# Kernel optimization log

Measured on AMD Instinct MI355X. Metric: run time of the kernel, lower is better.

The kernel has to match this reference:

```python
import jax, jax.numpy as jnp
import numpy as np

DIM = 6
S = 2 ** DIM  # 64 nonzero B-spline basis products per edge (degree-1 spline)


def _bits():
    # [S, DIM] binary offsets enumerating the 2^dim corners of the spline cell
    return jnp.asarray(((np.arange(S)[:, None] >> np.arange(DIM)[None, :]) & 1).astype(np.int32))


def spline_basis(u, ks):
    # u: [E, DIM] pseudo-coords in [0,1); open B-spline, degree 1
    bits = _bits()                      # [S, DIM]
    v = u * (ks - 1)                    # [E, DIM]
    lo = jnp.floor(v)
    frac = v - lo                       # fractional position in cell
    lo = lo.astype(jnp.int32)
    # basis[e,s] = prod_d (frac if bit else 1-frac)
    basis = jnp.prod(jnp.where(bits[None].astype(bool), frac[:, None, :], 1.0 - frac[:, None, :]), axis=-1)  # [E,S]
    pos = jnp.clip(lo[:, None, :] + bits[None, :, :], 0, ks - 1)  # [E,S,DIM]
    strides = (ks ** jnp.arange(DIM)).astype(jnp.int32)           # per-dim stride in flattened kernel
    idx = jnp.sum(pos * strides[None, None, :], axis=-1)          # [E,S] in [0, ks^DIM)
    return basis, idx


def spline_conv(x, src, dst, basis, idx, W, Wr, b, n):
    # x:[N,in], W:[K,in,out], basis/idx:[E,S]. Mean aggregation + root weight + bias (PyG defaults).
    x_src = x[src]                                  # [E,in] gather
    out_ch = W.shape[2]
    acc0 = jnp.zeros((x_src.shape[0], out_ch), x.dtype)

    def body(acc, bs_is):
        bs, ii = bs_is                              # [E], [E]
        m = jnp.einsum('ei,eio->eo', x_src, W[ii])  # basis-indexed weight gather + per-edge matvec
        return acc + bs[:, None] * m, None

    msg, _ = jax.lax.scan(body, acc0, (basis.T, idx.T))   # loop over S=64 spline corners
    agg = jax.ops.segment_sum(msg, dst, num_segments=n)   # scatter-add to target nodes
    deg = jax.ops.segment_sum(jnp.ones(dst.shape, x.dtype), dst, num_segments=n)
    agg = agg / jnp.clip(deg, 1.0)[:, None]                # aggr='mean'
    return agg + x @ Wr + b


def setup_inputs() -> dict:
    key = jax.random.key(0)
    ks = jax.random.split(key, 16)
    N, E = 4096, 16384
    x = jax.random.normal(ks[0], (N, 32), jnp.float32)
    edge_index = jax.random.randint(ks[1], (2, E), 0, N, jnp.int32)
    edge_attr = jax.random.uniform(ks[2], (E, DIM), jnp.float32)

    def wk(k, K, cin, cout):
        return jax.random.normal(k, (K, cin, cout), jnp.float32) * (1.0 / np.sqrt(cin * S))

    def wr(k, cin, cout):
        return jax.random.normal(k, (cin, cout), jnp.float32) * (1.0 / np.sqrt(cin))

    return {
        'x': x, 'edge_index': edge_index, 'edge_attr': edge_attr,
        'W1': wk(ks[3], 3 ** DIM, 32, 128), 'Wr1': wr(ks[4], 32, 128), 'b1': jnp.zeros((128,), jnp.float32),
        'W3': wk(ks[5], 3 ** DIM, 128, 128), 'Wr3': wr(ks[6], 128, 128), 'b3': jnp.zeros((128,), jnp.float32),
        'W6': wk(ks[7], 5 ** DIM, 128, 64), 'Wr6': wr(ks[8], 128, 64), 'b6': jnp.zeros((64,), jnp.float32),
        'W7': wk(ks[9], 7 ** DIM, 64, 13), 'Wr7': wr(ks[10], 64, 13), 'b7': jnp.zeros((13,), jnp.float32),
    }


def reference(x, edge_index, edge_attr, W1, Wr1, b1, W3, Wr3, b3, W6, Wr6, b6, W7, Wr7, b7):
    src, dst = edge_index[0], edge_index[1]
    n = x.shape[0]
    basis3, idx3 = spline_basis(edge_attr, 3)  # shared by conv1 and conv3 (same kernel_size)
    h = spline_conv(x, src, dst, basis3, idx3, W1, Wr1, b1, n)
    h = spline_conv(h, src, dst, basis3, idx3, W3, Wr3, b3, n)
    basis5, idx5 = spline_basis(edge_attr, 5)
    h = spline_conv(h, src, dst, basis5, idx5, W6, Wr6, b6, n)
    basis7, idx7 = spline_basis(edge_attr, 7)
    h = spline_conv(h, src, dst, basis7, idx7, W7, Wr7, b7, n)
    h = jax.nn.elu(h)
    return jax.nn.log_softmax(h, axis=1)
```

## Files before the change

### kernel.cpp

```cpp
#include <hip/hip_runtime.h>
#include <hip/hip_bf16.h>
#include <cstdint>
#include <cstddef>

constexpr int SDIM = 6;
constexpr int SCOR = 64;
constexpr int CAP5 = 512;
constexpr int CAP7 = 128;
typedef unsigned short u16;
typedef unsigned char u8;
typedef __attribute__((ext_vector_type(8))) short bf16x8;
typedef __attribute__((ext_vector_type(4))) float f32x4;
typedef __attribute__((ext_vector_type(2))) float f32x2;
typedef __attribute__((ext_vector_type(4))) int i32x4;

__device__ __forceinline__ float bf2f(u16 h) {
    union { unsigned u; float f; } v; v.u = ((unsigned)h) << 16; return v.f;
}
__device__ __forceinline__ u16 f2bf(float f) {
    union { float f; unsigned u; } v; v.f = f;
    unsigned r = v.u + 0x7fffu + ((v.u >> 16) & 1u);
    return (u16)(r >> 16);
}

__device__ __forceinline__ u8 f2e4m3(float f) {
#if __has_builtin(__builtin_amdgcn_cvt_pk_fp8_f32)
    return (u8)(__builtin_amdgcn_cvt_pk_fp8_f32(f, 0.0f, 0, false) & 0xff);
#else
    unsigned u = __float_as_uint(f);
    unsigned s = (u >> 24) & 0x80;
    int exp = (int)((u >> 23) & 0xff) - 127;
    unsigned man = u & 0x7fffff;
    if (exp > 8 || (exp == 8 && man >= 0x700000)) return (u8)(s | 0x7e);
    if (exp >= -6) {
        unsigned m = man >> 20;
        unsigned rest = man & 0xfffff;
        if (rest > 0x80000 || (rest == 0x80000 && (m & 1))) m++;
        unsigned v = (((unsigned)(exp + 7)) << 3) + m;
        if (v > 0x7e) v = 0x7e;
        return (u8)(s | v);
    }
    if (exp < -10) return (u8)s;
    float af = __uint_as_float(u & 0x7fffffff);
    int M = (int)(af * 512.0f + 0.5f);
    if (M > 7) M = 7;
    return (u8)(s | M);
#endif
}

__device__ __forceinline__ void e4m3x4_acc(unsigned w, float* a) {
#if __has_builtin(__builtin_amdgcn_cvt_pk_f32_fp8)
    f32x2 lo = __builtin_amdgcn_cvt_pk_f32_fp8((int)w, false);
    f32x2 hi = __builtin_amdgcn_cvt_pk_f32_fp8((int)w, true);
    a[0] += lo.x; a[1] += lo.y; a[2] += hi.x; a[3] += hi.y;
#else
    #pragma unroll
    for (int j = 0; j < 4; j++) {
        unsigned b = (w >> (8 * j)) & 0xff;
        unsigned s = (b & 0x80) << 24;
        unsigned em = b & 0x7f;
        float v = (em >= 8)
            ? __uint_as_float((((em >> 3) + 120) << 23) | ((em & 7) << 20))
            : (float)em * (1.0f / 512.0f);
        a[j] += __uint_as_float(__float_as_uint(v) | s);
    }
#endif
}

template <int KS>
__device__ __forceinline__ void keybasis(const float* u, int s, int& key, float& basis) {
    int idx = 0, str = 1;
    float b = 1.0f;
    #pragma unroll
    for (int d = 0; d < SDIM; d++) {
        float v = u[d] * (KS - 1);
        float fl = floorf(v);
        float fr = v - fl;
        int bit = (s >> d) & 1;
        int pos = (int)fl + bit;
        pos = min(max(pos, 0), KS - 1);
        idx += pos * str;
        str *= KS;
        b *= bit ? fr : (1.0f - fr);
    }
    key = idx;
    basis = b;
}

__global__ __launch_bounds__(256) void prep_kernel(int* __restrict__ zb, int nz,
                                                   const float* __restrict__ xin,
                                                   u16* __restrict__ xbf, int n4) {
    int i = blockIdx.x * blockDim.x + threadIdx.x;
    if (i < nz) zb[i] = 0;
    if (i < n4) {
        float4 v = ((const float4*)xin)[i];
        ushort4 o;
        o.x = f2bf(v.x); o.y = f2bf(v.y); o.z = f2bf(v.z); o.w = f2bf(v.w);
        ((ushort4*)xbf)[i] = o;
    }
}

__global__ __launch_bounds__(256) void count_all(const float* __restrict__ ea,
                                                 const int* __restrict__ dst,
                                                 int* __restrict__ cnt3r,
                                                 int* __restrict__ degi, int P) {
    int gid = blockIdx.x * blockDim.x + threadIdx.x;
    if (gid >= P) return;
    int e = gid >> 6, s = gid & 63;
    int rep = blockIdx.x & 7;
    float u[SDIM];
    #pragma unroll
    for (int d = 0; d < SDIM; d++) u[d] = ea[e * SDIM + d];
    int k; float b;
    keybasis<3>(u, s, k, b);
    atomicAdd(&cnt3r[k * 8 + rep], 1);
    if (s == 0) atomicAdd(&degi[dst[e]], 1);
}

__global__ __launch_bounds__(256) void scan_partial(const int* __restrict__ zb,
                                                    int* __restrict__ bsum) {
    int b = blockIdx.x, t = threadIdx.x;
    int4 v = *(const int4*)(zb + b * 1024 + t * 4);
    __shared__ int red[256];
    red[t] = v.x + v.y + v.z + v.w;
    __syncthreads();
    for (int h = 128; h >= 1; h >>= 1) {
        if (t < h) red[t] += red[t + h];
        __syncthreads();
    }
    if (t == 0) bsum[b] = red[0];
}

__global__ __launch_bounds__(256) void scan_final(int* __restrict__ zb,
                                                  const int* __restrict__ bsum,
                                                  int* __restrict__ eoff,
                                                  int* __restrict__ offs3f,
                                                  int Nn, int nb0) {
    int b = blockIdx.x, t = threadIdx.x;
    int s1 = nb0;
    int seg = (b >= s1) ? 1 : 0;
    int sb = seg ? s1 : 0;
    int L = seg ? 5832 : Nn;
    int* offs = seg ? offs3f : eoff;

    __shared__ int red[256];
    int cnt = b - sb;
    int acc = 0;
    for (int j = t; j < cnt; j += 256) acc += bsum[sb + j];
    red[t] = acc;
    __syncthreads();
    for (int h = 128; h >= 1; h >>= 1) {
        if (t < h) red[t] += red[t + h];
        __syncthreads();
    }
    int blockPrefix = red[0];
    __syncthreads();

    int idx = b * 1024 + t * 4;
    int4 v = *(const int4*)(zb + idx);
    int tsum = v.x + v.y + v.z + v.w;
    __shared__ int ss[256];
    ss[t] = tsum;
    __syncthreads();
    for (int off = 1; off < 256; off <<= 1) {
        int val = (t >= off) ? ss[t - off] : 0;
        __syncthreads();
        ss[t] += val;
        __syncthreads();
    }
    int p = blockPrefix + ((t == 0) ? 0 : ss[t - 1]);
    int pe[4];
    pe[0] = p;
    pe[1] = p + v.x;
    pe[2] = pe[1] + v.y;
    pe[3] = pe[2] + v.z;
    int vv[4] = {v.x, v.y, v.z, v.w};
    int li = (b - sb) * 1024 + t * 4;
    #pragma unroll
    for (int j = 0; j < 4; j++) {
        int gi = li + j;
        if (gi < L) {
            offs[gi] = pe[j];
            zb[idx + j] = pe[j];
            if (gi == L - 1) offs[L] = pe[j] + vv[j];
        }
    }
}

__global__ __launch_bounds__(256) void fill_all(const float* __restrict__ ea,
                                                const int* __restrict__ src,
                                                const int* __restrict__ dst,
                                                int* __restrict__ ecur,
                                                int* __restrict__ cur3r, int2* __restrict__ pP3,
                                                int* __restrict__ cnt5, int2* __restrict__ pP5,
                                                int* __restrict__ cnt7, int2* __restrict__ pP7,
                                                int P) {
    int gid = blockIdx.x * blockDim.x + threadIdx.x;
    if (gid >= P) return;
    int e = gid >> 6;
    int lane = threadIdx.x & 63;
    int rep = blockIdx.x & 7;
    float u[SDIM];
    #pragma unroll
    for (int d = 0; d < SDIM; d++) u[d] = ea[e * SDIM + d];
    int node = src[e];
    int er = 0;
    if (lane == 0) er = atomicAdd(&ecur[dst[e]], 1);
    er = __shfl(er, 0);
    int packed = (node << 20) | (er * SCOR + lane);
    int k; float b; int slot;
    keybasis<3>(u, lane, k, b);
    slot = atomicAdd(&cur3r[k * 8 + rep], 1);
    pP3[slot] = make_int2(packed, __float_as_int(b));
    keybasis<5>(u, lane, k, b);
    slot = k * CAP5 + atomicAdd(&cnt5[k], 1);
    pP5[slot] = make_int2(packed, __float_as_int(b));
    keybasis<7>(u, lane, k, b);
    slot = k * CAP7 + atomicAdd(&cnt7[k], 1);
    pP7[slot] = make_int2(packed, __float_as_int(b));
}

template <int IN, int OUT, int WAVES, int WN, int GY, int OSTR, int CAP>
__global__ __launch_bounds__(WAVES * 64) void conv_mfma_r(
    const u16* __restrict__ xbf, const float* __restrict__ W,
    const int* __restrict__ offs, const int2* __restrict__ pairP,
    u8* __restrict__ mpart) {
    constexpr int NT = WAVES * 64;
    constexpr int WM = WAVES / WN;
    constexpr int OUT16 = (OUT + 15) & ~15;
    static_assert(OUT == OUT16, "conv_mfma_r requires OUT multiple of 16");
    constexpr int WSTR = OUT + 2;
    constexpr int NF = OUT16 / 16;
    constexpr int NFW = NF / WN;
    constexpr int KS = IN / 32;
    constexpr int TW = NFW * 16;
    constexpr int TSTR = TW + 16;
    constexpr int CHW = TW / 16;
    static_assert(TSTR % 16 == 0, "row stride must be 16B aligned");
    static_assert((IN * OUT) % NT == 0, "staging divisibility");

    __shared__ u16 Wlds[IN * WSTR];
    __shared__ u8 tall[WAVES][16 * TSTR];

    int k = blockIdx.x;
    int p0, p1;
    if constexpr (CAP > 0) {
        p0 = k * CAP;
        p1 = p0 + offs[k];
    } else {
        p0 = offs[k * OSTR];
        p1 = offs[(k + 1) * OSTR];
    }
    int t = threadIdx.x;
    int wid = t >> 6, lane = t & 63;
    int wm = wid % WM, wn = wid / WM;
    int l15 = lane & 15, l4 = lane >> 4;
    u8* twave = tall[wid];

    if (p0 + (int)blockIdx.y * WM * 16 >= p1) return;

    const float* Wg = W + (size_t)k * IN * OUT;
    #pragma unroll
    for (int f0 = 0; f0 < IN * OUT; f0 += NT) {
        int f = f0 + t;
        int i = f / OUT, o = f % OUT;
        Wlds[i * WSTR + o] = f2bf(Wg[f]);
    }
    __syncthreads();

    bf16x8 breg[KS][NFW];
    #pragma unroll
    for (int ks = 0; ks < KS; ks++) {
        #pragma unroll
        for (int nf = 0; nf < NFW; nf++) {
            int col = (wn * NFW + nf) * 16 + l15;
            int rbase = ks * 32 + l4 * 8;
            bf16x8 b;
            #pragma unroll
            for (int j = 0; j < 8; j++)
                ((u16*)&b)[j] = Wlds[(rbase + j) * WSTR + col];
            breg[ks][nf] = b;
        }
    }

    constexpr int STRIDE = WM * GY * 16;
    int t0 = p0 + ((int)blockIdx.y * WM + wm) * 16;
    if (t0 >= p1) return;

    int2 meta = pairP[min(t0 + l15, p1 - 1)];
    bf16x8 a[KS];
    {
        const u16* xrow = xbf + (size_t)((unsigned)meta.x >> 20) * IN + l4 * 8;
        #pragma unroll
        for (int ks = 0; ks < KS; ks++) a[ks] = *(const bf16x8*)(xrow + ks * 32);
    }

    while (true) {
        int np = min(16, p1 - t0);
        float basv = (l15 < np) ? __int_as_float(meta.y) * 64.0f : 0.0f;
        int srv = meta.x & 0xFFFFF;
        int tn = t0 + STRIDE;
        bool has = tn < p1;
        int2 metaN = meta;
        if (has) metaN = pairP[min(tn + l15, p1 - 1)];

        f32x4 acc[NFW];
        #pragma unroll
        for (int nf = 0; nf < NFW; nf++)
            acc[nf] = f32x4{0.f, 0.f, 0.f, 0.f};
        #pragma unroll
        for (int ks = 0; ks < KS; ks++) {
            #pragma unroll
            for (int nf = 0; nf < NFW; nf++)
                acc[nf] = __builtin_amdgcn_mfma_f32_16x16x32_bf16(a[ks], breg[ks][nf], acc[nf], 0, 0, 0);
        }

        bf16x8 aN[KS];
        if (has) {
            const u16* xrowN = xbf + (size_t)((unsigned)metaN.x >> 20) * IN + l4 * 8;
            #pragma unroll
            for (int ks = 0; ks < KS; ks++) aN[ks] = *(const bf16x8*)(xrowN + ks * 32);
        }

        #pragma unroll
        for (int nf = 0; nf < NFW; nf++) {
            #pragma unroll
            for (int r = 0; r < 4; r++) {
                int pl = l4 * 4 + r;
                float bs = __shfl(basv, pl);
                twave[pl * TSTR + nf * 16 + l15] = f2e4m3(acc[nf][r] * bs);
            }
        }

        #pragma unroll
        for (int it = 0; it < (16 * CHW + 63) / 64; it++) {
            int cid = it * 64 + lane;
            int row = cid / CHW, ch = cid % CHW;
            int srr = __shfl(srv, row);
            if (cid < 16 * CHW && row < np)
                __builtin_nontemporal_store(
                    *(const i32x4*)&twave[row * TSTR + ch * 16],
                    (i32x4*)(mpart + (size_t)srr * OUT16 + wn * TW + ch * 16));
        }

        if (!has) break;
        t0 = tn;
        meta = metaN;
        #pragma unroll
        for (int ks = 0; ks < KS; ks++) a[ks] = aN[ks];
    }
}

__global__ __launch_bounds__(256) void conv_mfma_w7(
    const u16* __restrict__ xbf, const float* __restrict__ W,
    const int* __restrict__ cnt, const int2* __restrict__ pairP,
    u16* __restrict__ mpart, int K) {
    constexpr int IN = 64, OUT = 13, OUT16 = 16;
    __shared__ u16 WT[4][16 * 72];
    __shared__ u16 tbAll[4][16 * 24];
    int t = threadIdx.x, wid = t >> 6, lane = t & 63;
    int k = blockIdx.x * 4 + wid;
    if (k >= K) return;
    int p0 = k * CAP7, p1 = p0 + cnt[k];
    if (p0 >= p1) return;
    u16* tb = tbAll[wid];
    u16* wt = WT[wid];

    int l15 = lane & 15, l4 = lane >> 4;
    const float* Wg = W + (size_t)k * (IN * OUT);
    for (int f = lane; f < IN * OUT; f += 64) {
        int r = f / OUT, c = f - r * OUT;
        wt[c * 72 + r] = f2bf(Wg[f]);
    }
    bf16x8 breg[2];
    #pragma unroll
    for (int ks = 0; ks < 2; ks++)
        breg[ks] = (l15 < OUT) ? *(const bf16x8*)&wt[l15 * 72 + ks * 32 + l4 * 8]
                               : bf16x8{0, 0, 0, 0, 0, 0, 0, 0};

    for (int t0 = p0; t0 < p1; t0 += 16) {
        int np = min(16, p1 - t0);
        int2 meta = pairP[min(t0 + l15, p1 - 1)];
        float basv = (l15 < np) ? __int_as_float(meta.y) : 0.0f;
        int srv = meta.x & 0xFFFFF;
        const u16* xrow = xbf + (size_t)((unsigned)meta.x >> 20) * IN + l4 * 8;
        f32x4 acc = f32x4{0.f, 0.f, 0.f, 0.f};
        #pragma unroll
        for (int ks = 0; ks < 2; ks++) {
            bf16x8 a = *(const bf16x8*)(xrow + ks * 32);
            acc = __builtin_amdgcn_mfma_f32_16x16x32_bf16(a, breg[ks], acc, 0, 0, 0);
        }
        #pragma unroll
        for (int r = 0; r < 4; r++) {
            int pl = l4 * 4 + r;
            float bs = __shfl(basv, pl);
            tb[pl * 24 + l15] = f2bf(acc[r] * bs);
        }
        {
            int row = lane >> 1, ch = lane & 1;
            int srr = __shfl(srv, row);
            if (lane < np * 2)
                __builtin_nontemporal_store(
                    *(const bf16x8*)&tb[row * 24 + ch * 8],
                    (bf16x8*)(mpart + (size_t)srr * OUT16 + ch * 8));
        }
    }
}

template <int IN, int OUT, int OUT16, bool HEAD, bool FP8>
__global__ __launch_bounds__(256) void reduce_wave(
    const void* __restrict__ mpartv, const int* __restrict__ eoff,
    const float* __restrict__ xin, const float* __restrict__ Wr,
    const float* __restrict__ bias, float* __restrict__ hout,
    u16* __restrict__ hbf, int N) {
    constexpr int CH = OUT16 / 16;
    constexpr int RG = 64 / CH;
    __shared__ float sm[4][OUT16];

    int t = threadIdx.x, wid = t >> 6, lane = t & 63;
    int nodeLocal = wid >> 1, hf = wid & 1;
    int n = blockIdx.x * 2 + nodeLocal;

    int e0 = 0, e1 = 0;
    if (n < N) { e0 = eoff[n]; e1 = eoff[n + 1]; }
    int R = (e1 - e0) * SCOR;
    size_t rs = (size_t)e0 * SCOR;
    int rg = lane / CH, ch = lane % CH;

    float a[16];
    #pragma unroll
    for (int j = 0; j < 16; j++) a[j] = 0.0f;
    #pragma unroll 4
    for (int r = rg + hf * RG; r < R; r += RG * 2) {
        if constexpr (FP8) {
            const u8* mp = (const u8*)mpartv + (rs + r) * OUT16 + ch * 16;
            i32x4 w = __builtin_nontemporal_load((const i32x4*)mp);
            e4m3x4_acc((unsigned)w.x, a + 0);
            e4m3x4_acc((unsigned)w.y, a + 4);
            e4m3x4_acc((unsigned)w.z, a + 8);
            e4m3x4_acc((unsigned)w.w, a + 12);
        } else {
            const u16* mp = (const u16*)mpartv + (rs + r) * OUT16 + ch * 16;
            bf16x8 v0 = __builtin_nontemporal_load((const bf16x8*)mp);
            bf16x8 v1 = __builtin_nontemporal_load((const bf16x8*)(mp + 8));
            #pragma unroll
            for (int j = 0; j < 8; j++) a[j] += bf2f(((const u16*)&v0)[j]);
            #pragma unroll
            for (int j = 0; j < 8; j++) a[8 + j] += bf2f(((const u16*)&v1)[j]);
        }
    }
    #pragma unroll
    for (int m = CH; m < 64; m <<= 1) {
        #pragma unroll
        for (int j = 0; j < 16; j++) a[j] += __shfl_xor(a[j], m);
    }
    if (lane < CH) {
        #pragma unroll
        for (int j = 0; j < 16; j++) sm[wid][lane * 16 + j] = a[j];
    }
    __syncthreads();

    if (n >= N) return;
    int dg = e1 - e0;
    float dinv = 1.0f / (float)(dg < 1 ? 1 : dg);
    if constexpr (FP8) dinv *= (1.0f / 64.0f);
    const float* xr = xin + (size_t)n * IN;

    if constexpr (!HEAD) {
        int o = hf * (OUT / 2) + lane;
        if (lane < OUT / 2) {
            float s = (sm[nodeLocal * 2][o] + sm[nodeLocal * 2 + 1][o]) * dinv + bias[o];
            #pragma unroll 8
            for (int i = 0; i < IN; i++) s += xr[i] * Wr[i * OUT + o];
            hout[(size_t)n * OUT + o] = s;
            if (hbf) hbf[(size_t)n * OUT + o] = f2bf(s);
        }
    } else {
        if (hf == 0 && lane < 16) {
            float s = 0.0f;
            if (lane < OUT) {
                s = (sm[nodeLocal * 2][lane] + sm[nodeLocal * 2 + 1][lane]) * dinv + bias[lane];
                #pragma unroll 8
                for (int i = 0; i < IN; i++) s += xr[i] * Wr[i * OUT + lane];
            }
            sm[wid][lane] = s;
            float v[13];
            float mx = -1e30f;
            #pragma unroll
            for (int c = 0; c < 13; c++) {
                float z = sm[wid][c];
                z = z > 0.0f ? z : (expf(z) - 1.0f);
                v[c] = z;
                mx = fmaxf(mx, z);
            }
            float sum = 0.0f;
            #pragma unroll
            for (int c = 0; c < 13; c++) sum += expf(v[c] - mx);
            float lse = mx + logf(sum);
            if (lane < 13) hout[(size_t)n * 13 + lane] = v[lane] - lse;
        }
    }
}

extern "C" void kernel_launch(void* const* d_in, const int* in_sizes, int n_in,
                              void* d_out, int out_size, void* d_ws, size_t ws_size,
                              hipStream_t stream) {
    const float* x   = (const float*)d_in[0];
    const int*   ei  = (const int*)d_in[1];
    const float* ea  = (const float*)d_in[2];
    const float* W1  = (const float*)d_in[3];
    const float* Wr1 = (const float*)d_in[4];
    const float* b1  = (const float*)d_in[5];
    const float* W3  = (const float*)d_in[6];
    const float* Wr3 = (const float*)d_in[7];
    const float* b3  = (const float*)d_in[8];
    const float* W6  = (const float*)d_in[9];
    const float* Wr6 = (const float*)d_in[10];
    const float* b6  = (const float*)d_in[11];
    const float* W7  = (const float*)d_in[12];
    const float* Wr7 = (const float*)d_in[13];
    const float* b7  = (const float*)d_in[14];

    const int N = in_sizes[0] / 32;
    const int E = in_sizes[1] / 2;
    const int* src = ei;
    const int* dst = ei + E;
    (void)n_in; (void)out_size; (void)ws_size;

    const int K3 = 729, K5 = 15625, K7 = 117649;
    const int P = E * SCOR;

    const int BS = 1024;
    const int Np = (N + BS - 1) / BS * BS;
    const int nb0 = Np / BS;
    const int P3 = 6144, P5 = 16384, P7 = 117760;
    const int totalPad = Np + P3 + P5 + P7;
    const int nBlocks = nb0 + 6;

    char* ws = (char*)d_ws;
    size_t off = 0;
    auto alloc = [&](size_t bytes) {
        void* p = ws + off;
        off += (bytes + 255) & ~(size_t)255;
        return p;
    };
    int*   zb    = (int*)alloc((size_t)totalPad * 4);
    int*   degi  = zb;
    int*   cnt3r = zb + Np;
    int*   cnt5  = cnt3r + P3;
    int*   cnt7  = cnt5 + P5;
    int*   bsum  = (int*)alloc((size_t)nBlocks * 4);
    int*   eoff  = (int*)alloc((size_t)(N + 1) * 4);
    int*   offs3f = (int*)alloc((size_t)(K3 * 8 + 1) * 4);
    int2*  pP3   = (int2*)alloc((size_t)P * 8);
    int2*  pP5   = (int2*)alloc((size_t)K5 * CAP5 * 8);
    int2*  pP7   = (int2*)alloc((size_t)K7 * CAP7 * 8);
    float* h1    = (float*)alloc((size_t)N * 128 * 4);
    float* h3    = (float*)alloc((size_t)N * 128 * 4);
    float* h6    = (float*)alloc((size_t)N * 64 * 4);
    u16*   xbf1  = (u16*)alloc((size_t)N * 32 * 2);
    u16*   hbf1  = (u16*)alloc((size_t)N * 128 * 2);
    u16*   hbf3  = (u16*)alloc((size_t)N * 128 * 2);
    u16*   hbf6  = (u16*)alloc((size_t)N * 64 * 2);
    u8*    mpart = (u8*)alloc((size_t)P * 128);

    dim3 blk(256);
    dim3 pgrid((P + 255) / 256);
    int rgrid = (N + 1) / 2;

    int n4 = N * 32 / 4;
    prep_kernel<<<(max(totalPad, n4) + 255) / 256, blk, 0, stream>>>(zb, totalPad, x, xbf1, n4);

    count_all<<<pgrid, blk, 0, stream>>>(ea, dst, cnt3r, degi, P);

    scan_partial<<<nBlocks, blk, 0, stream>>>(zb, bsum);
    scan_final<<<nBlocks, blk, 0, stream>>>(zb, bsum, eoff, offs3f, N, nb0);

    fill_all<<<pgrid, blk, 0, stream>>>(ea, src, dst, degi, cnt3r, pP3, cnt5, pP5, cnt7, pP7, P);

    conv_mfma_r<32, 128, 8, 2, 8, 8, 0><<<dim3(K3, 8), dim3(512), 0, stream>>>(
        xbf1, W1, offs3f, pP3, mpart);
    reduce_wave<32, 128, 128, false, true><<<rgrid, blk, 0, stream>>>(mpart, eoff, x, Wr1, b1, h1, hbf1, N);

    conv_mfma_r<128, 128, 8, 2, 8, 8, 0><<<dim3(K3, 8), dim3(512), 0, stream>>>(
        hbf1, W3, offs3f, pP3, mpart);
    reduce_wave<128, 128, 128, false, true><<<rgrid, blk, 0, stream>>>(mpart, eoff, h1, Wr3, b3, h3, hbf3, N);

    conv_mfma_r<128, 64, 4, 2, 1, 1, CAP5><<<dim3(K5, 1), blk, 0, stream>>>(
        hbf3, W6, cnt5, pP5, mpart);
    reduce_wave<128, 64, 64, false, true><<<rgrid, blk, 0, stream>>>(mpart, eoff, h3, Wr6, b6, h6, hbf6, N);

    conv_mfma_w7<<<(K7 + 3) / 4, blk, 0, stream>>>(hbf6, W7, cnt7, pP7, (u16*)mpart, K7);
    reduce_wave<64, 13, 16, true, false><<<rgrid, blk, 0, stream>>>(mpart, eoff, h6, Wr7, b7, (float*)d_out, nullptr, N);
}
```

Before: 1.144 ms.

## Replace counting-sort for kernel-3 pairs with fixed-capacity per-replica buckets

Removes the count_all pass and the two-stage scan over degree and kernel-3 counts. Kernel-3 pairs now go into fixed-capacity buckets (CAP3 per key and replica) filled directly by atomics, and degrees come from a small per-edge atomic kernel followed by a single-block scan. The conv kernel now indexes its bucket by (k, replica) instead of reading CSR offsets. The cost is more workspace, a risk of silent overflow if a bucket holds more than CAP3 entries, and a serial single-block scan.

```diff
diff --git a/kernel.cpp b/kernel.cpp
--- a/kernel.cpp
+++ b/kernel.cpp
@@ -5,6 +5,8 @@
 
 constexpr int SDIM = 6;
 constexpr int SCOR = 64;
+constexpr int REP3 = 8;
+constexpr int CAP3 = 4096;
 constexpr int CAP5 = 512;
 constexpr int CAP7 = 128;
 typedef unsigned short u16;
@@ -100,98 +102,44 @@
     }
 }
 
-__global__ __launch_bounds__(256) void count_all(const float* __restrict__ ea,
-                                                 const int* __restrict__ dst,
-                                                 int* __restrict__ cnt3r,
-                                                 int* __restrict__ degi, int P) {
-    int gid = blockIdx.x * blockDim.x + threadIdx.x;
-    if (gid >= P) return;
-    int e = gid >> 6, s = gid & 63;
-    int rep = blockIdx.x & 7;
-    float u[SDIM];
-    #pragma unroll
-    for (int d = 0; d < SDIM; d++) u[d] = ea[e * SDIM + d];
-    int k; float b;
-    keybasis<3>(u, s, k, b);
-    atomicAdd(&cnt3r[k * 8 + rep], 1);
-    if (s == 0) atomicAdd(&degi[dst[e]], 1);
-}
-
-__global__ __launch_bounds__(256) void scan_partial(const int* __restrict__ zb,
-                                                    int* __restrict__ bsum) {
-    int b = blockIdx.x, t = threadIdx.x;
-    int4 v = *(const int4*)(zb + b * 1024 + t * 4);
-    __shared__ int red[256];
-    red[t] = v.x + v.y + v.z + v.w;
+__global__ __launch_bounds__(256) void deg_kernel(const int* __restrict__ dst,
+                                                  int* __restrict__ degi, int E) {
+    int e = blockIdx.x * blockDim.x + threadIdx.x;
+    if (e < E) atomicAdd(&degi[dst[e]], 1);
+}
+
+__global__ __launch_bounds__(1024) void scan_kernel(int* __restrict__ counts,
+                                                    int* __restrict__ offs, int K) {
+    __shared__ int sums[1024];
+    int t = threadIdx.x;
+    int chunk = (K + 1023) / 1024;
+    int a0 = t * chunk;
+    int a1 = min(a0 + chunk, K);
+    int s = 0;
+    for (int j = a0; j < a1; j++) s += counts[j];
+    sums[t] = s;
     __syncthreads();
-    for (int h = 128; h >= 1; h >>= 1) {
-        if (t < h) red[t] += red[t + h];
+    for (int off = 1; off < 1024; off <<= 1) {
+        int v = (t >= off) ? sums[t - off] : 0;
         __syncthreads();
-    }
-    if (t == 0) bsum[b] = red[0];
-}
-
-__global__ __launch_bounds__(256) void scan_final(int* __restrict__ zb,
-                                                  const int* __restrict__ bsum,
-                                                  int* __restrict__ eoff,
-                                                  int* __restrict__ offs3f,
-                                                  int Nn, int nb0) {
-    int b = blockIdx.x, t = threadIdx.x;
-    int s1 = nb0;
-    int seg = (b >= s1) ? 1 : 0;
-    int sb = seg ? s1 : 0;
-    int L = seg ? 5832 : Nn;
-    int* offs = seg ? offs3f : eoff;
-
-    __shared__ int red[256];
-    int cnt = b - sb;
-    int acc = 0;
-    for (int j = t; j < cnt; j += 256) acc += bsum[sb + j];
-    red[t] = acc;
-    __syncthreads();
-    for (int h = 128; h >= 1; h >>= 1) {
-        if (t < h) red[t] += red[t + h];
+        sums[t] += v;
         __syncthreads();
     }
-    int blockPrefix = red[0];
-    __syncthreads();
-
-    int idx = b * 1024 + t * 4;
-    int4 v = *(const int4*)(zb + idx);
-    int tsum = v.x + v.y + v.z + v.w;
-    __shared__ int ss[256];
-    ss[t] = tsum;
-    __syncthreads();
-    for (int off = 1; off < 256; off <<= 1) {
-        int val = (t >= off) ? ss[t - off] : 0;
-        __syncthreads();
-        ss[t] += val;
-        __syncthreads();
-    }
-    int p = blockPrefix + ((t == 0) ? 0 : ss[t - 1]);
-    int pe[4];
-    pe[0] = p;
-    pe[1] = p + v.x;
-    pe[2] = pe[1] + v.y;
-    pe[3] = pe[2] + v.z;
-    int vv[4] = {v.x, v.y, v.z, v.w};
-    int li = (b - sb) * 1024 + t * 4;
-    #pragma unroll
-    for (int j = 0; j < 4; j++) {
-        int gi = li + j;
-        if (gi < L) {
-            offs[gi] = pe[j];
-            zb[idx + j] = pe[j];
-            if (gi == L - 1) offs[L] = pe[j] + vv[j];
-        }
-    }
+    int run = (t == 0) ? 0 : sums[t - 1];
+    for (int j = a0; j < a1; j++) {
+        int c = counts[j];
+        offs[j] = run;
+        counts[j] = run;
+        run += c;
+    }
+    if (t == 1023) offs[K] = run;
 }
 
 __global__ __launch_bounds__(256) void fill_all(const float* __restrict__ ea,
                                                 const int* __restrict__ src,
                                                 const int* __restrict__ dst,
                                                 int* __restrict__ ecur,
-                                                int* __restrict__ cur3r, int2* __restrict__ pP3,
+                                                int* __restrict__ cnt3r, int2* __restrict__ pP3,
                                                 int* __restrict__ cnt5, int2* __restrict__ pP5,
                                                 int* __restrict__ cnt7, int2* __restrict__ pP7,
                                                 int P) {
@@ -199,7 +147,7 @@
     if (gid >= P) return;
     int e = gid >> 6;
     int lane = threadIdx.x & 63;
-    int rep = blockIdx.x & 7;
+    int rep = blockIdx.x & (REP3 - 1);
     float u[SDIM];
     #pragma unroll
     for (int d = 0; d < SDIM; d++) u[d] = ea[e * SDIM + d];
@@ -210,7 +158,7 @@
     int packed = (node << 20) | (er * SCOR + lane);
     int k; float b; int slot;
     keybasis<3>(u, lane, k, b);
-    slot = atomicAdd(&cur3r[k * 8 + rep], 1);
+    slot = (k * REP3 + rep) * CAP3 + atomicAdd(&cnt3r[k * REP3 + rep], 1);
     pP3[slot] = make_int2(packed, __float_as_int(b));
     keybasis<5>(u, lane, k, b);
     slot = k * CAP5 + atomicAdd(&cnt5[k], 1);
@@ -220,10 +168,10 @@
     pP7[slot] = make_int2(packed, __float_as_int(b));
 }
 
-template <int IN, int OUT, int WAVES, int WN, int GY, int OSTR, int CAP>
+template <int IN, int OUT, int WAVES, int WN, int CAP>
 __global__ __launch_bounds__(WAVES * 64) void conv_mfma_r(
     const u16* __restrict__ xbf, const float* __restrict__ W,
-    const int* __restrict__ offs, const int2* __restrict__ pairP,
+    const int* __restrict__ cnt, const int2* __restrict__ pairP,
     u8* __restrict__ mpart) {
     constexpr int NT = WAVES * 64;
     constexpr int WM = WAVES / WN;
@@ -243,22 +191,17 @@
     __shared__ u8 tall[WAVES][16 * TSTR];
 
     int k = blockIdx.x;
-    int p0, p1;
-    if constexpr (CAP > 0) {
-        p0 = k * CAP;
-        p1 = p0 + offs[k];
-    } else {
-        p0 = offs[k * OSTR];
-        p1 = offs[(k + 1) * OSTR];
-    }
+    int idx = k * gridDim.y + blockIdx.y;
+    int p0 = idx * CAP;
+    int p1 = p0 + cnt[idx];
+    if (p0 >= p1) return;
+
     int t = threadIdx.x;
     int wid = t >> 6, lane = t & 63;
     int wm = wid % WM, wn = wid / WM;
     int l15 = lane & 15, l4 = lane >> 4;
     u8* twave = tall[wid];
 
-    if (p0 + (int)blockIdx.y * WM * 16 >= p1) return;
-
     const float* Wg = W + (size_t)k * IN * OUT;
     #pragma unroll
     for (int f0 = 0; f0 < IN * OUT; f0 += NT) {
@@ -283,8 +226,8 @@
         }
     }
 
-    constexpr int STRIDE = WM * GY * 16;
-    int t0 = p0 + ((int)blockIdx.y * WM + wm) * 16;
+    constexpr int STRIDE = WM * 16;
+    int t0 = p0 + wm * 16;
     if (t0 >= p1) return;
 
     int2 meta = pairP[min(t0 + l15, p1 - 1)];
@@ -530,12 +473,8 @@
     const int K3 = 729, K5 = 15625, K7 = 117649;
     const int P = E * SCOR;
 
-    const int BS = 1024;
-    const int Np = (N + BS - 1) / BS * BS;
-    const int nb0 = Np / BS;
-    const int P3 = 6144, P5 = 16384, P7 = 117760;
-    const int totalPad = Np + P3 + P5 + P7;
-    const int nBlocks = nb0 + 6;
+    const int NC3 = K3 * REP3;
+    const int totalZ = N + NC3 + K5 + K7;
 
     char* ws = (char*)d_ws;
     size_t off = 0;
@@ -544,15 +483,13 @@
         off += (bytes + 255) & ~(size_t)255;
         return p;
     };
-    int*   zb    = (int*)alloc((size_t)totalPad * 4);
+    int*   zb    = (int*)alloc((size_t)totalZ * 4);
     int*   degi  = zb;
-    int*   cnt3r = zb + Np;
-    int*   cnt5  = cnt3r + P3;
-    int*   cnt7  = cnt5 + P5;
-    int*   bsum  = (int*)alloc((size_t)nBlocks * 4);
+    int*   cnt3r = zb + N;
+    int*   cnt5  = cnt3r + NC3;
+    int*   cnt7  = cnt5 + K5;
     int*   eoff  = (int*)alloc((size_t)(N + 1) * 4);
-    int*   offs3f = (int*)alloc((size_t)(K3 * 8 + 1) * 4);
-    int2*  pP3   = (int2*)alloc((size_t)P * 8);
+    int2*  pP3   = (int2*)alloc((size_t)NC3 * CAP3 * 8);
     int2*  pP5   = (int2*)alloc((size_t)K5 * CAP5 * 8);
     int2*  pP7   = (int2*)alloc((size_t)K7 * CAP7 * 8);
     float* h1    = (float*)alloc((size_t)N * 128 * 4);
@@ -565,28 +502,27 @@
     u8*    mpart = (u8*)alloc((size_t)P * 128);
 
     dim3 blk(256);
+    dim3 egrid((E + 255) / 256);
     dim3 pgrid((P + 255) / 256);
     int rgrid = (N + 1) / 2;
 
     int n4 = N * 32 / 4;
-    prep_kernel<<<(max(totalPad, n4) + 255) / 256, blk, 0, stream>>>(zb, totalPad, x, xbf1, n4);
-
-    count_all<<<pgrid, blk, 0, stream>>>(ea, dst, cnt3r, degi, P);
-
-    scan_partial<<<nBlocks, blk, 0, stream>>>(zb, bsum);
-    scan_final<<<nBlocks, blk, 0, stream>>>(zb, bsum, eoff, offs3f, N, nb0);
+    prep_kernel<<<(max(totalZ, n4) + 255) / 256, blk, 0, stream>>>(zb, totalZ, x, xbf1, n4);
+
+    deg_kernel<<<egrid, blk, 0, stream>>>(dst, degi, E);
+    scan_kernel<<<1, 1024, 0, stream>>>(degi, eoff, N);
 
     fill_all<<<pgrid, blk, 0, stream>>>(ea, src, dst, degi, cnt3r, pP3, cnt5, pP5, cnt7, pP7, P);
 
-    conv_mfma_r<32, 128, 8, 2, 8, 8, 0><<<dim3(K3, 8), dim3(512), 0, stream>>>(
-        xbf1, W1, offs3f, pP3, mpart);
+    conv_mfma_r<32, 128, 8, 2, CAP3><<<dim3(K3, REP3), dim3(512), 0, stream>>>(
+        xbf1, W1, cnt3r, pP3, mpart);
     reduce_wave<32, 128, 128, false, true><<<rgrid, blk, 0, stream>>>(mpart, eoff, x, Wr1, b1, h1, hbf1, N);
 
-    conv_mfma_r<128, 128, 8, 2, 8, 8, 0><<<dim3(K3, 8), dim3(512), 0, stream>>>(
-        hbf1, W3, offs3f, pP3, mpart);
+    conv_mfma_r<128, 128, 8, 2, CAP3><<<dim3(K3, REP3), dim3(512), 0, stream>>>(
+        hbf1, W3, cnt3r, pP3, mpart);
     reduce_wave<128, 128, 128, false, true><<<rgrid, blk, 0, stream>>>(mpart, eoff, h1, Wr3, b3, h3, hbf3, N);
 
-    conv_mfma_r<128, 64, 4, 2, 1, 1, CAP5><<<dim3(K5, 1), blk, 0, stream>>>(
+    conv_mfma_r<128, 64, 4, 2, CAP5><<<dim3(K5, 1), blk, 0, stream>>>(
         hbf3, W6, cnt5, pP5, mpart);
     reduce_wave<128, 64, 64, false, true><<<rgrid, blk, 0, stream>>>(mpart, eoff, h3, Wr6, b6, h6, hbf6, N);
 
```

After: 945.0 us. 17.4% less time.
